# Kernel optimization log

Hardware: AMD Instinct MI355X
Metric: run time of the kernel (lower is better)

## Reference

```python
import jax, jax.numpy as jnp
import numpy as np

B, S, D, H = 16, 1024, 768, 12
Dh = D // H  # 64


def setup_inputs() -> dict:
    key = jax.random.key(0)
    ks = jax.random.split(key, 7)
    return {
        "tokens": jax.random.normal(ks[0], (B, S, D), dtype=jnp.float32),
        "Wq": jax.random.normal(ks[1], (H, Dh, Dh), dtype=jnp.float32) * (1.0 / np.sqrt(Dh)),
        "bq": jax.random.normal(ks[2], (H, Dh), dtype=jnp.float32) * 0.02,
        "Wk": jax.random.normal(ks[3], (H, Dh, Dh), dtype=jnp.float32) * (1.0 / np.sqrt(Dh)),
        "bk": jax.random.normal(ks[4], (H, Dh), dtype=jnp.float32) * 0.02,
        "Wv": jax.random.normal(ks[5], (H, Dh, Dh), dtype=jnp.float32) * (1.0 / np.sqrt(Dh)),
        "bv": jax.random.normal(ks[6], (H, Dh), dtype=jnp.float32) * 0.02,
    }


def reference(tokens, Wq, bq, Wk, bk, Wv, bv):
    b, s, d = tokens.shape
    h, dh = Wq.shape[0], Wq.shape[1]
    x = tokens.reshape(b, s, h, dh)  # per-head slice of last dim, matches torch slicing
    # torch Linear: y = x @ W.T + b, per head. W stored as [h, out, in].
    q = jnp.einsum('bshd,hed->bshe', x, Wq) + bq  # [b,s,h,dh]
    k = jnp.einsum('bshd,hed->bshe', x, Wk) + bk
    v = jnp.einsum('bshd,hed->bshe', x, Wv) + bv
    scale = 1.0 / jnp.sqrt(jnp.asarray(dh, dtype=tokens.dtype))
    scores = jnp.einsum('bqhd,bkhd->bhqk', q, k) * scale  # [b,h,s,s]
    attn = jax.nn.softmax(scores, axis=-1)
    out = jnp.einsum('bhqk,bkhd->bqhd', attn, v)  # [b,s,h,dh]
    return out.reshape(b, s, d)  # hstack of heads == reshape since head axis contiguous
```

## Files before the change

kernel.cpp:

```cpp
#include <hip/hip_runtime.h>
#include <math.h>

#define NB 16
#define NS 1024
#define ND 768
#define NH 12
#define NDH 64

static constexpr size_t QKV_ELEMS = (size_t)NB * NH * NS * NDH;
static constexpr float QSCALE = 0.125f * 1.44269504088896f;

typedef __attribute__((ext_vector_type(8))) _Float16 half8;
typedef __attribute__((ext_vector_type(2))) _Float16 half2t;
typedef __attribute__((ext_vector_type(4))) float f32x4;

__device__ __forceinline__ void proj_one(
    const float* __restrict__ W, int h, int l16, int lg,
    const half8 xh[2][2], const half8 xl[2][2], f32x4 acc[2][4])
{
    #pragma unroll
    for (int n = 0; n < 4; ++n)
        #pragma unroll
        for (int kc = 0; kc < 2; ++kc) {
            const float* pw = W + (size_t)(h * NDH + n * 16 + l16) * NDH + kc * 32 + lg * 8;
            const float4 a = *reinterpret_cast<const float4*>(pw);
            const float4 b = *reinterpret_cast<const float4*>(pw + 4);
            const float wv[8] = {a.x, a.y, a.z, a.w, b.x, b.y, b.z, b.w};
            half8 wf;
            #pragma unroll
            for (int j = 0; j < 8; ++j) wf[j] = (_Float16)wv[j];
            #pragma unroll
            for (int m = 0; m < 2; ++m) {
                acc[m][n] = __builtin_amdgcn_mfma_f32_16x16x32_f16(xh[m][kc], wf, acc[m][n], 0, 0, 0);
                acc[m][n] = __builtin_amdgcn_mfma_f32_16x16x32_f16(xl[m][kc], wf, acc[m][n], 0, 0, 0);
            }
        }
}

__global__ __launch_bounds__(256) void qkv_mfma(
    const float* __restrict__ x,
    const float* __restrict__ Wq, const float* __restrict__ bq,
    const float* __restrict__ Wk, const float* __restrict__ bk,
    const float* __restrict__ Wv, const float* __restrict__ bv,
    _Float16* __restrict__ qo, _Float16* __restrict__ ko, _Float16* __restrict__ vT)
{
    const int tb = blockIdx.x;
    const int h  = blockIdx.y;
    const int t  = threadIdx.x;
    const int w  = t >> 6;
    const int l  = t & 63;
    const int l16 = l & 15, lg = l >> 4;
    const int tok0 = tb * 128 + w * 32;
    const int b  = tok0 >> 10;
    const int s0 = tok0 & 1023;
    const int bh = b * NH + h;

    half8 xh[2][2], xl[2][2];
    #pragma unroll
    for (int m = 0; m < 2; ++m)
        #pragma unroll
        for (int kc = 0; kc < 2; ++kc) {
            const float* px = x + (size_t)(tok0 + m * 16 + l16) * ND + h * NDH + kc * 32 + lg * 8;
            const float4 a = *reinterpret_cast<const float4*>(px);
            const float4 c = *reinterpret_cast<const float4*>(px + 4);
            const float vv[8] = {a.x, a.y, a.z, a.w, c.x, c.y, c.z, c.w};
            #pragma unroll
            for (int j = 0; j < 8; ++j) {
                const _Float16 hi = (_Float16)vv[j];
                xh[m][kc][j] = hi;
                xl[m][kc][j] = (_Float16)(vv[j] - (float)hi);
            }
        }

    f32x4 acc[2][4];

    #pragma unroll
    for (int m = 0; m < 2; ++m)
        #pragma unroll
        for (int n = 0; n < 4; ++n) acc[m][n] = f32x4{0.f, 0.f, 0.f, 0.f};
    proj_one(Wq, h, l16, lg, xh, xl, acc);
    #pragma unroll
    for (int n = 0; n < 4; ++n) {
        const float bb = bq[h * NDH + n * 16 + l16];
        #pragma unroll
        for (int m = 0; m < 2; ++m)
            #pragma unroll
            for (int r = 0; r < 4; ++r)
                qo[((size_t)bh * NS + s0 + m * 16 + lg * 4 + r) * NDH + n * 16 + l16] =
                    (_Float16)((acc[m][n][r] + bb) * QSCALE);
    }

    #pragma unroll
    for (int m = 0; m < 2; ++m)
        #pragma unroll
        for (int n = 0; n < 4; ++n) acc[m][n] = f32x4{0.f, 0.f, 0.f, 0.f};
    proj_one(Wk, h, l16, lg, xh, xl, acc);
    #pragma unroll
    for (int n = 0; n < 4; ++n) {
        const float bb = bk[h * NDH + n * 16 + l16];
        #pragma unroll
        for (int m = 0; m < 2; ++m)
            #pragma unroll
            for (int r = 0; r < 4; ++r)
                ko[((size_t)bh * NS + s0 + m * 16 + lg * 4 + r) * NDH + n * 16 + l16] =
                    (_Float16)(acc[m][n][r] + bb);
    }

    #pragma unroll
    for (int m = 0; m < 2; ++m)
        #pragma unroll
        for (int n = 0; n < 4; ++n) acc[m][n] = f32x4{0.f, 0.f, 0.f, 0.f};
    proj_one(Wv, h, l16, lg, xh, xl, acc);
    #pragma unroll
    for (int n = 0; n < 4; ++n) {
        const float bb = bv[h * NDH + n * 16 + l16];
        #pragma unroll
        for (int m = 0; m < 2; ++m)
            #pragma unroll
            for (int r = 0; r < 4; ++r)
                vT[((size_t)bh * NDH + n * 16 + l16) * NS + s0 + m * 16 + lg * 4 + r] =
                    (_Float16)(acc[m][n][r] + bb);
    }
}

__global__ __launch_bounds__(64) void flash_mfma(
    const _Float16* __restrict__ q, const _Float16* __restrict__ k,
    const _Float16* __restrict__ vT, float* __restrict__ out)
{
    __shared__ __align__(16) _Float16 PT[32 * 64];

    const int i   = blockIdx.x;
    const int xcd = i & 7;
    const int c   = i >> 3;
    const int bh  = xcd * 24 + (c >> 5);
    const int q0  = (c & 31) * 32;
    const int l   = threadIdx.x;
    const int l16 = l & 15, lg = l >> 4;

    const size_t qkbase = (size_t)bh * NS * NDH;
    const size_t vtbase = (size_t)bh * NDH * NS;

    half8 qf[2][2];
    #pragma unroll
    for (int n2 = 0; n2 < 2; ++n2)
        #pragma unroll
        for (int kc = 0; kc < 2; ++kc)
            qf[n2][kc] = *reinterpret_cast<const half8*>(
                q + qkbase + (size_t)(q0 + n2 * 16 + l16) * NDH + kc * 32 + lg * 8);

    f32x4 Oacc[2][4];
    #pragma unroll
    for (int m = 0; m < 2; ++m)
        #pragma unroll
        for (int n = 0; n < 4; ++n) Oacc[m][n] = f32x4{0.f, 0.f, 0.f, 0.f};
    float mi[2] = {-INFINITY, -INFINITY};
    float li[2] = {0.f, 0.f};

    half8 kf[4][2];
    #pragma unroll
    for (int m4 = 0; m4 < 4; ++m4)
        #pragma unroll
        for (int kc = 0; kc < 2; ++kc)
            kf[m4][kc] = *reinterpret_cast<const half8*>(
                k + qkbase + (size_t)(m4 * 16 + l16) * NDH + kc * 32 + lg * 8);

    for (int kt = 0; kt < 16; ++kt) {
        const int kvb = kt * 64;

        half8 vf[4][2];
        #pragma unroll
        for (int n4 = 0; n4 < 4; ++n4)
            #pragma unroll
            for (int kc = 0; kc < 2; ++kc)
                vf[n4][kc] = *reinterpret_cast<const half8*>(
                    vT + vtbase + (size_t)(n4 * 16 + l16) * NS + kvb + kc * 32 + lg * 8);

        f32x4 st[4][2];
        #pragma unroll
        for (int m4 = 0; m4 < 4; ++m4)
            #pragma unroll
            for (int n2 = 0; n2 < 2; ++n2) {
                st[m4][n2] = f32x4{0.f, 0.f, 0.f, 0.f};
                #pragma unroll
                for (int kc = 0; kc < 2; ++kc)
                    st[m4][n2] = __builtin_amdgcn_mfma_f32_16x16x32_f16(
                        kf[m4][kc], qf[n2][kc], st[m4][n2], 0, 0, 0);
            }

        half8 kf2[4][2];
        if (kt < 15) {
            #pragma unroll
            for (int m4 = 0; m4 < 4; ++m4)
                #pragma unroll
                for (int kc = 0; kc < 2; ++kc)
                    kf2[m4][kc] = *reinterpret_cast<const half8*>(
                        k + qkbase + (size_t)(kvb + 64 + m4 * 16 + l16) * NDH + kc * 32 + lg * 8);
        }

        float cfac[2];
        #pragma unroll
        for (int n2 = 0; n2 < 2; ++n2) {
            float pm = st[0][n2][0];
            #pragma unroll
            for (int m4 = 0; m4 < 4; ++m4)
                #pragma unroll
                for (int r = 0; r < 4; ++r) pm = fmaxf(pm, st[m4][n2][r]);
            pm = fmaxf(pm, __shfl_xor(pm, 16));
            pm = fmaxf(pm, __shfl_xor(pm, 32));
            const float mn = fmaxf(mi[n2], pm);
            cfac[n2] = __builtin_amdgcn_exp2f(mi[n2] - mn);
            mi[n2] = mn;
            float rs = 0.f;
            #pragma unroll
            for (int m4 = 0; m4 < 4; ++m4)
                #pragma unroll
                for (int r = 0; r < 4; ++r) {
                    const float p = __builtin_amdgcn_exp2f(st[m4][n2][r] - mn);
                    st[m4][n2][r] = p;
                    rs += p;
                }
            rs += __shfl_xor(rs, 16);
            rs += __shfl_xor(rs, 32);
            li[n2] = li[n2] * cfac[n2] + rs;
        }

        #pragma unroll
        for (int m2 = 0; m2 < 2; ++m2) {
            float cb[4];
            #pragma unroll
            for (int r = 0; r < 4; ++r) cb[r] = __shfl(cfac[m2], lg * 4 + r);
            #pragma unroll
            for (int n4 = 0; n4 < 4; ++n4)
                #pragma unroll
                for (int r = 0; r < 4; ++r) Oacc[m2][n4][r] *= cb[r];
        }

        #pragma unroll
        for (int n2 = 0; n2 < 2; ++n2) {
            const int row = n2 * 16 + l16;
            #pragma unroll
            for (int m4 = 0; m4 < 4; ++m4) {
                const unsigned int p01 = __builtin_bit_cast(unsigned int,
                    __builtin_amdgcn_cvt_pkrtz(st[m4][n2][0], st[m4][n2][1]));
                const unsigned int p23 = __builtin_bit_cast(unsigned int,
                    __builtin_amdgcn_cvt_pkrtz(st[m4][n2][2], st[m4][n2][3]));
                const int swz = (m4 * 2 + (lg >> 1)) ^ (row & 7);
                uint2* dst = reinterpret_cast<uint2*>(&PT[row * 64 + swz * 8 + (lg & 1) * 4]);
                *dst = uint2{p01, p23};
            }
        }

        half8 pf[2][2];
        #pragma unroll
        for (int m2 = 0; m2 < 2; ++m2) {
            const int row = m2 * 16 + l16;
            #pragma unroll
            for (int kc = 0; kc < 2; ++kc) {
                const int swz = (kc * 4 + lg) ^ (row & 7);
                pf[m2][kc] = *reinterpret_cast<const half8*>(&PT[row * 64 + swz * 8]);
            }
        }

        #pragma unroll
        for (int m2 = 0; m2 < 2; ++m2)
            #pragma unroll
            for (int n4 = 0; n4 < 4; ++n4)
                #pragma unroll
                for (int kc = 0; kc < 2; ++kc)
                    Oacc[m2][n4] = __builtin_amdgcn_mfma_f32_16x16x32_f16(
                        pf[m2][kc], vf[n4][kc], Oacc[m2][n4], 0, 0, 0);

        #pragma unroll
        for (int m4 = 0; m4 < 4; ++m4)
            #pragma unroll
            for (int kc = 0; kc < 2; ++kc) kf[m4][kc] = kf2[m4][kc];
    }

    const int b = bh / NH;
    const int h = bh % NH;
    float inv[2] = {1.f / li[0], 1.f / li[1]};
    #pragma unroll
    for (int m2 = 0; m2 < 2; ++m2)
        #pragma unroll
        for (int r = 0; r < 4; ++r) {
            const float ib = __shfl(inv[m2], lg * 4 + r);
            const int s = q0 + m2 * 16 + lg * 4 + r;
            #pragma unroll
            for (int n4 = 0; n4 < 4; ++n4)
                out[((size_t)b * NS + s) * ND + h * NDH + n4 * 16 + l16] = Oacc[m2][n4][r] * ib;
        }
}

extern "C" void kernel_launch(void* const* d_in, const int* in_sizes, int n_in,
                              void* d_out, int out_size, void* d_ws, size_t ws_size,
                              hipStream_t stream)
{
    const float* x  = (const float*)d_in[0];
    const float* Wq = (const float*)d_in[1];
    const float* bq = (const float*)d_in[2];
    const float* Wk = (const float*)d_in[3];
    const float* bk = (const float*)d_in[4];
    const float* Wv = (const float*)d_in[5];
    const float* bv = (const float*)d_in[6];
    float* out = (float*)d_out;

    _Float16* qb = (_Float16*)d_ws;
    _Float16* kb = qb + QKV_ELEMS;
    _Float16* vt = kb + QKV_ELEMS;

    dim3 g1(NB * NS / 128, NH);
    qkv_mfma<<<g1, 256, 0, stream>>>(x, Wq, bq, Wk, bk, Wv, bv, qb, kb, vt);

    flash_mfma<<<NB * NH * 32, 64, 0, stream>>>(qb, kb, vt, out);
}
```

Measured before the change: 325.2 us.

## Use 4-wave flash blocks, MFMA priority hints, and transposed V projection

The flash attention kernel now runs 256-thread blocks with four waves, each owning 32 query rows and a private LDS tile, on a 2D grid indexed by (batch·head, query tile). This replaces single-wave blocks with an XCD-aware index mapping, so waves of the same head share a block and can reuse K/V through cache. s_setprio is raised around the MFMA sections so compute-heavy waves get issue priority. The V projection computes the transposed product directly (W as the A operand), so vT stores run contiguous along sequence, but the explicit XCD-locality remap is lost.

```diff
diff --git a/kernel.cpp b/kernel.cpp
--- a/kernel.cpp
+++ b/kernel.cpp
@@ -11,7 +11,6 @@
 static constexpr float QSCALE = 0.125f * 1.44269504088896f;
 
 typedef __attribute__((ext_vector_type(8))) _Float16 half8;
-typedef __attribute__((ext_vector_type(2))) _Float16 half2t;
 typedef __attribute__((ext_vector_type(4))) float f32x4;
 
 __device__ __forceinline__ void proj_one(
@@ -106,36 +105,53 @@
                     (_Float16)(acc[m][n][r] + bb);
     }
 
-    #pragma unroll
-    for (int m = 0; m < 2; ++m)
-        #pragma unroll
-        for (int n = 0; n < 4; ++n) acc[m][n] = f32x4{0.f, 0.f, 0.f, 0.f};
-    proj_one(Wv, h, l16, lg, xh, xl, acc);
-    #pragma unroll
-    for (int n = 0; n < 4; ++n) {
-        const float bb = bv[h * NDH + n * 16 + l16];
-        #pragma unroll
-        for (int m = 0; m < 2; ++m)
-            #pragma unroll
-            for (int r = 0; r < 4; ++r)
-                vT[((size_t)bh * NDH + n * 16 + l16) * NS + s0 + m * 16 + lg * 4 + r] =
-                    (_Float16)(acc[m][n][r] + bb);
-    }
+    f32x4 accT[4][2];
+    #pragma unroll
+    for (int dt = 0; dt < 4; ++dt)
+        #pragma unroll
+        for (int tt = 0; tt < 2; ++tt) accT[dt][tt] = f32x4{0.f, 0.f, 0.f, 0.f};
+    #pragma unroll
+    for (int dt = 0; dt < 4; ++dt)
+        #pragma unroll
+        for (int kc = 0; kc < 2; ++kc) {
+            const float* pw = Wv + (size_t)(h * NDH + dt * 16 + l16) * NDH + kc * 32 + lg * 8;
+            const float4 a = *reinterpret_cast<const float4*>(pw);
+            const float4 b = *reinterpret_cast<const float4*>(pw + 4);
+            const float wv[8] = {a.x, a.y, a.z, a.w, b.x, b.y, b.z, b.w};
+            half8 wf;
+            #pragma unroll
+            for (int j = 0; j < 8; ++j) wf[j] = (_Float16)wv[j];
+            #pragma unroll
+            for (int tt = 0; tt < 2; ++tt) {
+                accT[dt][tt] = __builtin_amdgcn_mfma_f32_16x16x32_f16(wf, xh[tt][kc], accT[dt][tt], 0, 0, 0);
+                accT[dt][tt] = __builtin_amdgcn_mfma_f32_16x16x32_f16(wf, xl[tt][kc], accT[dt][tt], 0, 0, 0);
+            }
+        }
+    #pragma unroll
+    for (int dt = 0; dt < 4; ++dt)
+        #pragma unroll
+        for (int r = 0; r < 4; ++r) {
+            const float bb = bv[h * NDH + dt * 16 + lg * 4 + r];
+            #pragma unroll
+            for (int tt = 0; tt < 2; ++tt)
+                vT[((size_t)bh * NDH + dt * 16 + lg * 4 + r) * NS + s0 + tt * 16 + l16] =
+                    (_Float16)(accT[dt][tt][r] + bb);
+        }
 }
 
-__global__ __launch_bounds__(64) void flash_mfma(
+__global__ __launch_bounds__(256, 4) void flash_mfma(
     const _Float16* __restrict__ q, const _Float16* __restrict__ k,
     const _Float16* __restrict__ vT, float* __restrict__ out)
 {
-    __shared__ __align__(16) _Float16 PT[32 * 64];
-
-    const int i   = blockIdx.x;
-    const int xcd = i & 7;
-    const int c   = i >> 3;
-    const int bh  = xcd * 24 + (c >> 5);
-    const int q0  = (c & 31) * 32;
-    const int l   = threadIdx.x;
+    __shared__ __align__(16) _Float16 PT[4][32 * 64];
+
+    const int bh = blockIdx.x;
+    const int qt = blockIdx.y;
+    const int t  = threadIdx.x;
+    const int w  = t >> 6;
+    const int l  = t & 63;
     const int l16 = l & 15, lg = l >> 4;
+    const int q0 = qt * 128 + w * 32;
 
     const size_t qkbase = (size_t)bh * NS * NDH;
     const size_t vtbase = (size_t)bh * NDH * NS;
@@ -176,6 +192,7 @@
                     vT + vtbase + (size_t)(n4 * 16 + l16) * NS + kvb + kc * 32 + lg * 8);
 
         f32x4 st[4][2];
+        __builtin_amdgcn_s_setprio(1);
         #pragma unroll
         for (int m4 = 0; m4 < 4; ++m4)
             #pragma unroll
@@ -186,6 +203,7 @@
                     st[m4][n2] = __builtin_amdgcn_mfma_f32_16x16x32_f16(
                         kf[m4][kc], qf[n2][kc], st[m4][n2], 0, 0, 0);
             }
+        __builtin_amdgcn_s_setprio(0);
 
         half8 kf2[4][2];
         if (kt < 15) {
@@ -235,6 +253,7 @@
                 for (int r = 0; r < 4; ++r) Oacc[m2][n4][r] *= cb[r];
         }
 
+        _Float16* Pw = PT[w];
         #pragma unroll
         for (int n2 = 0; n2 < 2; ++n2) {
             const int row = n2 * 16 + l16;
@@ -245,7 +264,7 @@
                 const unsigned int p23 = __builtin_bit_cast(unsigned int,
                     __builtin_amdgcn_cvt_pkrtz(st[m4][n2][2], st[m4][n2][3]));
                 const int swz = (m4 * 2 + (lg >> 1)) ^ (row & 7);
-                uint2* dst = reinterpret_cast<uint2*>(&PT[row * 64 + swz * 8 + (lg & 1) * 4]);
+                uint2* dst = reinterpret_cast<uint2*>(&Pw[row * 64 + swz * 8 + (lg & 1) * 4]);
                 *dst = uint2{p01, p23};
             }
         }
@@ -257,10 +276,11 @@
             #pragma unroll
             for (int kc = 0; kc < 2; ++kc) {
                 const int swz = (kc * 4 + lg) ^ (row & 7);
-                pf[m2][kc] = *reinterpret_cast<const half8*>(&PT[row * 64 + swz * 8]);
-            }
-        }
-
+                pf[m2][kc] = *reinterpret_cast<const half8*>(&Pw[row * 64 + swz * 8]);
+            }
+        }
+
+        __builtin_amdgcn_s_setprio(1);
         #pragma unroll
         for (int m2 = 0; m2 < 2; ++m2)
             #pragma unroll
@@ -269,6 +289,7 @@
                 for (int kc = 0; kc < 2; ++kc)
                     Oacc[m2][n4] = __builtin_amdgcn_mfma_f32_16x16x32_f16(
                         pf[m2][kc], vf[n4][kc], Oacc[m2][n4], 0, 0, 0);
+        __builtin_amdgcn_s_setprio(0);
 
         #pragma unroll
         for (int m4 = 0; m4 < 4; ++m4)
@@ -311,5 +332,6 @@
     dim3 g1(NB * NS / 128, NH);
     qkv_mfma<<<g1, 256, 0, stream>>>(x, Wq, bq, Wk, bk, Wv, bv, qb, kb, vt);
 
-    flash_mfma<<<NB * NH * 32, 64, 0, stream>>>(qb, kb, vt, out);
+    dim3 g2(NB * NH, 8);
+    flash_mfma<<<g2, 256, 0, stream>>>(qb, kb, vt, out);
 }
```

After: 571.4 us. 1.76x slower.
